# Kernel optimization log

Hardware: AMD Instinct MI355X
Metric: run time of the kernel (lower is better)

The kernel has to match this reference:

```python
import jax, jax.numpy as jnp
import numpy as np

N_NODES = 50000
N_EDGES = 400000
N_GRAPHS = 512
F = 32        # num_features
NB = 32       # mp_num_basis_fn
ZMAX = 118
CUTOFF = 5.0
NSPH = 9      # (mp_max_degree+1)^2 with max_degree=2
DEG_IDX = jnp.array([0, 1, 1, 1, 2, 2, 2, 2, 2])  # degree of each spherical component


def _bernstein(u, n=NB):
    # reciprocal_bernstein radial basis: Bernstein polynomials of degree n-1 at u in [0,1)
    k = jnp.arange(n, dtype=jnp.float32)
    log_binom = (jax.scipy.special.gammaln(float(n)) - jax.scipy.special.gammaln(k + 1.0)
                 - jax.scipy.special.gammaln(float(n) - k))
    u = jnp.clip(u, 1e-7, 1.0 - 1e-7)[..., None]
    return jnp.exp(log_binom + k * jnp.log(u) + (float(n) - 1.0 - k) * jnp.log1p(-u))


def _smooth_cutoff(r, cutoff=CUTOFF):
    t = r / cutoff
    return jnp.where(t < 1.0, jnp.exp(1.0 - 1.0 / jnp.clip(1.0 - t * t, 1e-7, None)), 0.0)


def _sph(u):
    # real spherical harmonics (cartesian normalization) up to degree 2; u: (E,3) unit vectors
    x, y, z = u[:, 0], u[:, 1], u[:, 2]
    c = jnp.sqrt(jnp.float32(3.0))
    return jnp.stack([jnp.ones_like(x), y, z, x,
                      c * x * y, c * y * z, 0.5 * (3.0 * z * z - 1.0),
                      c * z * x, 0.5 * c * (x * x - y * y)], axis=-1)


def _dense(x, W, b):
    # equivariant Dense: shared kernel over spherical components, bias only on scalar (l=0)
    y = jnp.einsum('nmf,fg->nmg', x, W)
    return y.at[:, 0, :].add(b)


def _silu_gate(x):
    # equivariant silu: scalar channel gates all degrees (scalar part -> exact silu)
    return x * jax.nn.sigmoid(x[:, 0:1, :])


def setup_inputs() -> dict:
    key = jax.random.key(0)
    ks = jax.random.split(key, 24)
    s = 1.0 / np.sqrt(F)
    sb = 1.0 / np.sqrt(NB)
    inp = {
        'positions': 2.0 * jax.random.normal(ks[0], (N_NODES, 3), jnp.float32),
        'embed': jax.random.normal(ks[1], (ZMAX, F), jnp.float32),
        'Wy0': sb * jax.random.normal(ks[2], (3, NB, F), jnp.float32),
        'Wx0': sb * jax.random.normal(ks[3], (3, NB, F), jnp.float32),
        'W1_0': s * jax.random.normal(ks[4], (F, F), jnp.float32),
        'b1_0': jnp.zeros((F,), jnp.float32),
        'W2_0': s * jax.random.normal(ks[5], (F, F), jnp.float32),
        'b2_0': jnp.zeros((F,), jnp.float32),
        'c0': jnp.full((1,), 0.5, jnp.float32),
        'Wr_last': sb * jax.random.normal(ks[6], (NB, F), jnp.float32),
        'W1_1': s * jax.random.normal(ks[7], (F, F), jnp.float32),
        'b1_1': jnp.zeros((F,), jnp.float32),
        'W2_1': s * jax.random.normal(ks[8], (F, F), jnp.float32),
        'b2_1': jnp.zeros((F,), jnp.float32),
        'c1': jnp.full((1,), 0.5, jnp.float32),
        'Wro1': s * jax.random.normal(ks[9], (F, F), jnp.float32),
        'bro1': jnp.zeros((F,), jnp.float32),
        'Wro2': s * jax.random.normal(ks[10], (F, 1), jnp.float32),
        'bro2': jnp.zeros((1,), jnp.float32),
        'atomic_bias': jax.random.normal(ks[11], (ZMAX,), jnp.float32),
        'atomic_numbers': jax.random.randint(ks[12], (N_NODES,), 0, ZMAX, jnp.int32),
        'dst_idx': jax.random.randint(ks[13], (N_EDGES,), 0, N_NODES, jnp.int32),
        'src_idx': jax.random.randint(ks[14], (N_EDGES,), 0, N_NODES, jnp.int32),
        'batch_segments': jnp.sort(jax.random.randint(ks[15], (N_NODES,), 0, N_GRAPHS, jnp.int32)),
        'graph_mask': jnp.ones((N_GRAPHS,), jnp.bool_),
    }
    return inp


def reference(positions, embed, Wy0, Wx0, W1_0, b1_0, W2_0, b2_0, c0,
              Wr_last, W1_1, b1_1, W2_1, b2_1, c1,
              Wro1, bro1, Wro2, bro2, atomic_bias,
              atomic_numbers, dst_idx, src_idx, batch_segments, graph_mask):
    # --- edge geometry (gather_src/gather_dst) ---
    disp = positions[src_idx] - positions[dst_idx]                # (E,3)
    r = jnp.sqrt(jnp.sum(disp * disp, axis=-1) + 1e-12)           # (E,)
    u = disp / r[:, None]
    Y = _sph(u)                                                   # (E,9)
    rbf = _bernstein(r / (r + 1.0)) * _smooth_cutoff(r)[:, None]  # (E,NB)

    # --- atomic embedding, lifted to (N, 9, F) with zero higher degrees ---
    x0 = embed[atomic_numbers]                                    # (N,F)
    x = jnp.concatenate([x0[:, None, :], jnp.zeros((N_NODES, NSPH - 1, F), x0.dtype)], axis=1)

    # --- iteration 0: full-degree equivariant message pass ---
    wy = jnp.einsum('eb,lbf->elf', rbf, Wy0)[:, DEG_IDX, :]       # (E,9,F) radial weights, (0,l)->l path
    wx = jnp.einsum('eb,lbf->elf', rbf, Wx0)[:, DEG_IDX, :]       # (l,0)->l path
    xs = x[src_idx]                                               # (E,9,F)
    msg = wy * Y[:, :, None] * xs[:, 0:1, :] + wx * xs
    y = jax.ops.segment_sum(msg, dst_idx, num_segments=N_NODES)   # (N,9,F)
    y = x + y
    y = _silu_gate(_dense(y, W1_0, b1_0))
    y = _dense(y, W2_0, b2_0)
    x = x + jax.nn.silu(c0) * y                                   # y_nl == 0 (era disabled)

    # --- iteration 1 (last): max_degree=0 message pass, then reduce to scalars ---
    w0 = rbf @ Wr_last                                            # (E,F)
    msg0 = w0 * x[src_idx, 0, :]
    y0 = jax.ops.segment_sum(msg0, dst_idx, num_segments=N_NODES) # (N,F)
    xs0 = x[:, 0, :]                                              # change_max_degree -> scalars
    y0 = xs0 + y0
    y0 = jax.nn.silu(y0 @ W1_1 + b1_1)
    y0 = y0 @ W2_1 + b2_1
    xs0 = xs0 + jax.nn.silu(c1) * y0

    # --- atomic readout and per-graph sum ---
    h = jax.nn.silu(xs0 @ Wro1 + bro1)
    e_atom = (h @ Wro2)[:, 0] + bro2[0] + atomic_bias[atomic_numbers]
    e_graph = jax.ops.segment_sum(e_atom, batch_segments, num_segments=N_GRAPHS)
    return jnp.where(graph_mask, e_graph, 0.0)
```

## Files before the change

kernel.cpp:

```cpp
#include <hip/hip_runtime.h>
#include <math.h>

#define NNODES 50000
#define NEDGES 400000
#define NGRAPHS 512
#define FDIM 32
#define CAP 32

static __device__ const float BINOM31[32] = {
    1.f, 31.f, 465.f, 4495.f, 31465.f, 169911.f, 736281.f, 2629575.f,
    7888725.f, 20160075.f, 44352165.f, 84672315.f, 141120525.f, 206253075.f,
    265182525.f, 300540195.f, 300540195.f, 265182525.f, 206253075.f,
    141120525.f, 84672315.f, 44352165.f, 20160075.f, 7888725.f, 2629575.f,
    736281.f, 169911.f, 31465.f, 4495.f, 465.f, 31.f, 1.f
};

__device__ __forceinline__ float fast_rcp(float x) {
    return __builtin_amdgcn_rcpf(x);
}
__device__ __forceinline__ float silu(float x) {
    return x * fast_rcp(1.0f + __expf(-x));
}

__global__ __launch_bounds__(256) void build_csr(
    const float* __restrict__ pos,
    const int* __restrict__ srci, const int* __restrict__ dsti,
    const int* __restrict__ Z,
    float4* __restrict__ pay, int* __restrict__ deg)
{
    int e = blockIdx.x * 256 + threadIdx.x;
    if (e >= NEDGES) return;
    int s = srci[e], d = dsti[e];
    float dx = pos[3 * s]     - pos[3 * d];
    float dy = pos[3 * s + 1] - pos[3 * d + 1];
    float dz = pos[3 * s + 2] - pos[3 * d + 2];
    float r = sqrtf(dx * dx + dy * dy + dz * dz + 1e-12f);
    if (r >= 5.0f) return;

    float t = r * 0.2f;
    float q = fmaxf(1.0f - t * t, 1e-7f);
    float cut = __expf(1.0f - fast_rcp(q));
    float v = fast_rcp(r + 1.0f);
    float v2 = v * v, v4 = v2 * v2, v8 = v4 * v4, v16 = v8 * v8;
    float scale = v16 * v8 * v4 * v2 * v * cut;

    int rank = atomicAdd(&deg[d], 1);
    if (rank < CAP)
        pay[(size_t)d * CAP + rank] =
            make_float4(r, scale,
                        __int_as_float(s * FDIM),
                        __int_as_float(Z[s] * FDIM));
}

#define GATHER_PIPE(ACC, XSRC, ROWSEL, CWL)                                \
    float ACC = 0.0f;                                                      \
    if (dgr > 0) {                                                         \
        float4 _pa = _h0, _pb = _h1;                                       \
        const float2* _cw = (const float2*)((CWL) + (f << 1));             \
        for (int j = 0; ; j += 2) {                                        \
            float _xa = (XSRC)[__float_as_int(_pa.ROWSEL) + f];            \
            float _xb = (XSRC)[__float_as_int(_pb.ROWSEL) + f];            \
            float4 _na = slot[j + 2];                                      \
            float4 _nb = slot[j + 3];                                      \
            float _r2a = _pa.x * _pa.x, _r2b = _pb.x * _pb.x;              \
            float2 _c15 = _cw[15 * 32];                                    \
            float _ea = _c15.x, _oa = _c15.y;                              \
            float _eb = _c15.x, _ob = _c15.y;                              \
            _Pragma("unroll")                                              \
            for (int p = 14; p >= 0; --p) {                                \
                float2 _cc = _cw[p * 32];                                  \
                _ea = fmaf(_ea, _r2a, _cc.x);                              \
                _oa = fmaf(_oa, _r2a, _cc.y);                              \
                _eb = fmaf(_eb, _r2b, _cc.x);                              \
                _ob = fmaf(_ob, _r2b, _cc.y);                              \
            }                                                              \
            float _wa = fmaf(_pa.x, _oa, _ea);                             \
            float _wb = fmaf(_pb.x, _ob, _eb);                             \
            ACC = fmaf(_pa.y * _wa, _xa, ACC);                             \
            ACC = fmaf(_pb.y * _wb, _xb, ACC);                             \
            if (j + 2 >= dgr) break;                                       \
            _pa = _na; _pb = _nb;                                          \
        }                                                                  \
    }

#define MATVEC32L(RES, WL, YP, BIAS) do {                                  \
    float4 _q0=(YP)[0], _q1=(YP)[1], _q2=(YP)[2], _q3=(YP)[3];             \
    float4 _q4=(YP)[4], _q5=(YP)[5], _q6=(YP)[6], _q7=(YP)[7];             \
    float _a0=(BIAS), _a1=0.f, _a2=0.f, _a3=0.f;                           \
    _a0=fmaf(_q0.x,(WL)[ 0*FDIM+f],_a0); _a0=fmaf(_q0.y,(WL)[ 1*FDIM+f],_a0); \
    _a0=fmaf(_q0.z,(WL)[ 2*FDIM+f],_a0); _a0=fmaf(_q0.w,(WL)[ 3*FDIM+f],_a0); \
    _a1=fmaf(_q1.x,(WL)[ 4*FDIM+f],_a1); _a1=fmaf(_q1.y,(WL)[ 5*FDIM+f],_a1); \
    _a1=fmaf(_q1.z,(WL)[ 6*FDIM+f],_a1); _a1=fmaf(_q1.w,(WL)[ 7*FDIM+f],_a1); \
    _a2=fmaf(_q2.x,(WL)[ 8*FDIM+f],_a2); _a2=fmaf(_q2.y,(WL)[ 9*FDIM+f],_a2); \
    _a2=fmaf(_q2.z,(WL)[10*FDIM+f],_a2); _a2=fmaf(_q2.w,(WL)[11*FDIM+f],_a2); \
    _a3=fmaf(_q3.x,(WL)[12*FDIM+f],_a3); _a3=fmaf(_q3.y,(WL)[13*FDIM+f],_a3); \
    _a3=fmaf(_q3.z,(WL)[14*FDIM+f],_a3); _a3=fmaf(_q3.w,(WL)[15*FDIM+f],_a3); \
    _a0=fmaf(_q4.x,(WL)[16*FDIM+f],_a0); _a0=fmaf(_q4.y,(WL)[17*FDIM+f],_a0); \
    _a0=fmaf(_q4.z,(WL)[18*FDIM+f],_a0); _a0=fmaf(_q4.w,(WL)[19*FDIM+f],_a0); \
    _a1=fmaf(_q5.x,(WL)[20*FDIM+f],_a1); _a1=fmaf(_q5.y,(WL)[21*FDIM+f],_a1); \
    _a1=fmaf(_q5.z,(WL)[22*FDIM+f],_a1); _a1=fmaf(_q5.w,(WL)[23*FDIM+f],_a1); \
    _a2=fmaf(_q6.x,(WL)[24*FDIM+f],_a2); _a2=fmaf(_q6.y,(WL)[25*FDIM+f],_a2); \
    _a2=fmaf(_q6.z,(WL)[26*FDIM+f],_a2); _a2=fmaf(_q6.w,(WL)[27*FDIM+f],_a2); \
    _a3=fmaf(_q7.x,(WL)[28*FDIM+f],_a3); _a3=fmaf(_q7.y,(WL)[29*FDIM+f],_a3); \
    _a3=fmaf(_q7.z,(WL)[30*FDIM+f],_a3); _a3=fmaf(_q7.w,(WL)[31*FDIM+f],_a3); \
    RES = (_a0+_a1)+(_a2+_a3); } while (0)

__global__ __launch_bounds__(256, 8) void fused_a(
    const float4* __restrict__ pay, const int* __restrict__ deg,
    const float* __restrict__ embed, const int* __restrict__ Z,
    const float* __restrict__ Wy0, const float* __restrict__ Wx0,
    const float* __restrict__ W1, const float* __restrict__ b1,
    const float* __restrict__ W2, const float* __restrict__ b2,
    const float* __restrict__ c0,
    float* __restrict__ x1buf)
{
    __shared__ __align__(16) float ylds[4][64];
    __shared__ __align__(16) float cwl[FDIM * FDIM];
    __shared__ __align__(16) float W1l[FDIM * FDIM];
    __shared__ __align__(16) float W2l[FDIM * FDIM];
    int tid = threadIdx.x;
    int widx = tid >> 6;
    int lane = tid & 63;
    int f    = lane & 31;
    int half = lane >> 5;

    int n = (blockIdx.x * 4 + widx) * 2 + half;
    const float4* slot = pay + (size_t)n * CAP;
    int dgr = (min(deg[n], CAP) + 1) & ~1;
    float4 _h0 = slot[0], _h1 = slot[1];
    float x0 = embed[Z[n] * FDIM + f];

    for (int i = tid; i < FDIM * FDIM; i += 256) {
        int k = i >> 5, ff = i & 31;
        cwl[(k >> 1) * 64 + (ff << 1) + (k & 1)] =
            BINOM31[k] * (Wy0[i] + Wx0[i]);
        W1l[i] = W1[i];
        W2l[i] = W2[i];
    }
    __syncthreads();

    GATHER_PIPE(accv, embed, w, cwl)

    float yv = x0 + accv;

    float* yrow = &ylds[widx][half * 32];
    const float4* yp = (const float4*)yrow;
    yrow[f] = yv;
    float t;
    MATVEC32L(t, W1l, yp, b1[f]);
    t = silu(t);
    yrow[f] = t;
    float u;
    MATVEC32L(u, W2l, yp, b2[f]);
    x1buf[(size_t)n * FDIM + f] = fmaf(silu(c0[0]), u, x0);
}

__global__ __launch_bounds__(256, 8) void fused_b(
    const float4* __restrict__ pay, const int* __restrict__ deg,
    const float* __restrict__ x1buf, const float* __restrict__ Wr_last,
    const float* __restrict__ W1, const float* __restrict__ b1,
    const float* __restrict__ W2, const float* __restrict__ b2,
    const float* __restrict__ c1,
    const float* __restrict__ Wro1, const float* __restrict__ bro1,
    const float* __restrict__ Wro2, const float* __restrict__ bro2,
    const float* __restrict__ abias, const int* __restrict__ Z,
    const int* __restrict__ segs,
    float* __restrict__ out)
{
    __shared__ __align__(16) float ylds[4][64];
    __shared__ __align__(16) float cwl[FDIM * FDIM];
    __shared__ __align__(16) float W1l[FDIM * FDIM];
    __shared__ __align__(16) float W2l[FDIM * FDIM];
    __shared__ __align__(16) float Wrl[FDIM * FDIM];
    __shared__ float eb[8];
    __shared__ int   sb[8];
    int tid = threadIdx.x;
    int widx = tid >> 6;
    int lane = tid & 63;
    int f    = lane & 31;
    int half = lane >> 5;

    int n = (blockIdx.x * 4 + widx) * 2 + half;
    const float4* slot = pay + (size_t)n * CAP;
    int dgr = (min(deg[n], CAP) + 1) & ~1;
    float4 _h0 = slot[0], _h1 = slot[1];
    float x1 = x1buf[(size_t)n * FDIM + f];
    int   zn = Z[n];

    for (int i = tid; i < FDIM * FDIM; i += 256) {
        int k = i >> 5, ff = i & 31;
        cwl[(k >> 1) * 64 + (ff << 1) + (k & 1)] = BINOM31[k] * Wr_last[i];
        W1l[i] = W1[i];
        W2l[i] = W2[i];
        Wrl[i] = Wro1[i];
    }
    __syncthreads();

    GATHER_PIPE(accv, x1buf, z, cwl)

    float yv = x1 + accv;

    float* yrow = &ylds[widx][half * 32];
    const float4* yp = (const float4*)yrow;
    yrow[f] = yv;
    float t;
    MATVEC32L(t, W1l, yp, b1[f]);
    t = silu(t);
    yrow[f] = t;
    float u;
    MATVEC32L(u, W2l, yp, b2[f]);
    float xs0 = fmaf(silu(c1[0]), u, x1);
    yrow[f] = xs0;
    float h;
    MATVEC32L(h, Wrl, yp, bro1[f]);
    float p = silu(h) * Wro2[f];
    p += __shfl_xor(p, 16, 32);
    p += __shfl_xor(p, 8, 32);
    p += __shfl_xor(p, 4, 32);
    p += __shfl_xor(p, 2, 32);
    p += __shfl_xor(p, 1, 32);

    if (f == 0) {
        eb[widx * 2 + half] = p + bro2[0] + abias[zn];
        sb[widx * 2 + half] = segs[n];
    }
    __syncthreads();
    if (tid == 0) {
        float acc = eb[0];
        int cur = sb[0];
        #pragma unroll
        for (int i = 1; i < 8; ++i) {
            if (sb[i] == cur) acc += eb[i];
            else { atomicAdd(&out[cur], acc); cur = sb[i]; acc = eb[i]; }
        }
        atomicAdd(&out[cur], acc);
    }
}

extern "C" void kernel_launch(void* const* d_in, const int* in_sizes, int n_in,
                              void* d_out, int out_size, void* d_ws, size_t ws_size,
                              hipStream_t stream)
{
    const float* pos     = (const float*)d_in[0];
    const float* embed   = (const float*)d_in[1];
    const float* Wy0     = (const float*)d_in[2];
    const float* Wx0     = (const float*)d_in[3];
    const float* W1_0    = (const float*)d_in[4];
    const float* b1_0    = (const float*)d_in[5];
    const float* W2_0    = (const float*)d_in[6];
    const float* b2_0    = (const float*)d_in[7];
    const float* c0      = (const float*)d_in[8];
    const float* Wr_last = (const float*)d_in[9];
    const float* W1_1    = (const float*)d_in[10];
    const float* b1_1    = (const float*)d_in[11];
    const float* W2_1    = (const float*)d_in[12];
    const float* b2_1    = (const float*)d_in[13];
    const float* c1      = (const float*)d_in[14];
    const float* Wro1    = (const float*)d_in[15];
    const float* bro1    = (const float*)d_in[16];
    const float* Wro2    = (const float*)d_in[17];
    const float* bro2    = (const float*)d_in[18];
    const float* abias   = (const float*)d_in[19];
    const int*   Z       = (const int*)d_in[20];
    const int*   dsti    = (const int*)d_in[21];
    const int*   srci    = (const int*)d_in[22];
    const int*   segs    = (const int*)d_in[23];

    float* out = (float*)d_out;

    char* w = (char*)d_ws;
    float4* pay   = (float4*)w;  w += (size_t)NNODES * CAP * 16;
    float*  x1buf = (float*)w;   w += (size_t)NNODES * FDIM * 4;
    int*    deg   = (int*)w;     w += (size_t)NNODES * 4;

    const int edgeBlocks = (NEDGES + 255) / 256;
    const int nodeBlocks = NNODES / 8;

    hipMemsetAsync(pay, 0, (size_t)NNODES * CAP * 16, stream);
    hipMemsetAsync(deg, 0, (size_t)NNODES * 4, stream);
    hipMemsetAsync(out, 0, (size_t)NGRAPHS * 4, stream);

    build_csr<<<edgeBlocks, 256, 0, stream>>>(pos, srci, dsti, Z, pay, deg);
    fused_a<<<nodeBlocks, 256, 0, stream>>>(pay, deg, embed, Z, Wy0, Wx0,
                                            W1_0, b1_0, W2_0, b2_0, c0, x1buf);
    fused_b<<<nodeBlocks, 256, 0, stream>>>(pay, deg, x1buf, Wr_last,
                                            W1_1, b1_1, W2_1, b2_1, c1,
                                            Wro1, bro1, Wro2, bro2,
                                            abias, Z, segs, out);
}
```

Baseline: 192.1 us.

## Make node kernels persistent with register-resident weights and in-loop segment accumulation

Result: no change. 189.2 us (-1.5%).

```diff
diff --git a/kernel.cpp b/kernel.cpp
--- a/kernel.cpp
+++ b/kernel.cpp
@@ -7,7 +7,11 @@
 #define FDIM 32
 #define CAP 32
 
-static __device__ const float BINOM31[32] = {
+#define NHALVES 4096
+#define NQ   (NNODES / NHALVES)
+#define NREM (NNODES % NHALVES)
+
+static constexpr float BINOM31[32] = {
     1.f, 31.f, 465.f, 4495.f, 31465.f, 169911.f, 736281.f, 2629575.f,
     7888725.f, 20160075.f, 44352165.f, 84672315.f, 141120525.f, 206253075.f,
     265182525.f, 300540195.f, 300540195.f, 265182525.f, 206253075.f,
@@ -52,27 +56,25 @@
                         __int_as_float(Z[s] * FDIM));
 }
 
-#define GATHER_PIPE(ACC, XSRC, ROWSEL, CWL)                                \
+#define GATHER_REG(ACC, XSRC, ROWSEL)                                      \
     float ACC = 0.0f;                                                      \
     if (dgr > 0) {                                                         \
-        float4 _pa = _h0, _pb = _h1;                                       \
-        const float2* _cw = (const float2*)((CWL) + (f << 1));             \
+        const float4* slot = pay + (size_t)n * CAP;                        \
+        float4 _pa = h0c, _pb = h1c;                                       \
         for (int j = 0; ; j += 2) {                                        \
             float _xa = (XSRC)[__float_as_int(_pa.ROWSEL) + f];            \
             float _xb = (XSRC)[__float_as_int(_pb.ROWSEL) + f];            \
             float4 _na = slot[j + 2];                                      \
             float4 _nb = slot[j + 3];                                      \
             float _r2a = _pa.x * _pa.x, _r2b = _pb.x * _pb.x;              \
-            float2 _c15 = _cw[15 * 32];                                    \
-            float _ea = _c15.x, _oa = _c15.y;                              \
-            float _eb = _c15.x, _ob = _c15.y;                              \
+            float _ea = cw[30], _oa = cw[31];                              \
+            float _eb = cw[30], _ob = cw[31];                              \
             _Pragma("unroll")                                              \
             for (int p = 14; p >= 0; --p) {                                \
-                float2 _cc = _cw[p * 32];                                  \
-                _ea = fmaf(_ea, _r2a, _cc.x);                              \
-                _oa = fmaf(_oa, _r2a, _cc.y);                              \
-                _eb = fmaf(_eb, _r2b, _cc.x);                              \
-                _ob = fmaf(_ob, _r2b, _cc.y);                              \
+                _ea = fmaf(_ea, _r2a, cw[2 * p]);                          \
+                _oa = fmaf(_oa, _r2a, cw[2 * p + 1]);                      \
+                _eb = fmaf(_eb, _r2b, cw[2 * p]);                          \
+                _ob = fmaf(_ob, _r2b, cw[2 * p + 1]);                      \
             }                                                              \
             float _wa = fmaf(_pa.x, _oa, _ea);                             \
             float _wb = fmaf(_pb.x, _ob, _eb);                             \
@@ -83,29 +85,35 @@
         }                                                                  \
     }
 
-#define MATVEC32L(RES, WL, YP, BIAS) do {                                  \
-    float4 _q0=(YP)[0], _q1=(YP)[1], _q2=(YP)[2], _q3=(YP)[3];             \
-    float4 _q4=(YP)[4], _q5=(YP)[5], _q6=(YP)[6], _q7=(YP)[7];             \
+#define MATVEC32R(RES, WR, BIAS) do {                                      \
+    float4 _q0=yp[0], _q1=yp[1], _q2=yp[2], _q3=yp[3];                     \
+    float4 _q4=yp[4], _q5=yp[5], _q6=yp[6], _q7=yp[7];                     \
     float _a0=(BIAS), _a1=0.f, _a2=0.f, _a3=0.f;                           \
-    _a0=fmaf(_q0.x,(WL)[ 0*FDIM+f],_a0); _a0=fmaf(_q0.y,(WL)[ 1*FDIM+f],_a0); \
-    _a0=fmaf(_q0.z,(WL)[ 2*FDIM+f],_a0); _a0=fmaf(_q0.w,(WL)[ 3*FDIM+f],_a0); \
-    _a1=fmaf(_q1.x,(WL)[ 4*FDIM+f],_a1); _a1=fmaf(_q1.y,(WL)[ 5*FDIM+f],_a1); \
-    _a1=fmaf(_q1.z,(WL)[ 6*FDIM+f],_a1); _a1=fmaf(_q1.w,(WL)[ 7*FDIM+f],_a1); \
-    _a2=fmaf(_q2.x,(WL)[ 8*FDIM+f],_a2); _a2=fmaf(_q2.y,(WL)[ 9*FDIM+f],_a2); \
-    _a2=fmaf(_q2.z,(WL)[10*FDIM+f],_a2); _a2=fmaf(_q2.w,(WL)[11*FDIM+f],_a2); \
-    _a3=fmaf(_q3.x,(WL)[12*FDIM+f],_a3); _a3=fmaf(_q3.y,(WL)[13*FDIM+f],_a3); \
-    _a3=fmaf(_q3.z,(WL)[14*FDIM+f],_a3); _a3=fmaf(_q3.w,(WL)[15*FDIM+f],_a3); \
-    _a0=fmaf(_q4.x,(WL)[16*FDIM+f],_a0); _a0=fmaf(_q4.y,(WL)[17*FDIM+f],_a0); \
-    _a0=fmaf(_q4.z,(WL)[18*FDIM+f],_a0); _a0=fmaf(_q4.w,(WL)[19*FDIM+f],_a0); \
-    _a1=fmaf(_q5.x,(WL)[20*FDIM+f],_a1); _a1=fmaf(_q5.y,(WL)[21*FDIM+f],_a1); \
-    _a1=fmaf(_q5.z,(WL)[22*FDIM+f],_a1); _a1=fmaf(_q5.w,(WL)[23*FDIM+f],_a1); \
-    _a2=fmaf(_q6.x,(WL)[24*FDIM+f],_a2); _a2=fmaf(_q6.y,(WL)[25*FDIM+f],_a2); \
-    _a2=fmaf(_q6.z,(WL)[26*FDIM+f],_a2); _a2=fmaf(_q6.w,(WL)[27*FDIM+f],_a2); \
-    _a3=fmaf(_q7.x,(WL)[28*FDIM+f],_a3); _a3=fmaf(_q7.y,(WL)[29*FDIM+f],_a3); \
-    _a3=fmaf(_q7.z,(WL)[30*FDIM+f],_a3); _a3=fmaf(_q7.w,(WL)[31*FDIM+f],_a3); \
+    _a0=fmaf(_q0.x,WR[ 0],_a0); _a0=fmaf(_q0.y,WR[ 1],_a0);                \
+    _a0=fmaf(_q0.z,WR[ 2],_a0); _a0=fmaf(_q0.w,WR[ 3],_a0);                \
+    _a1=fmaf(_q1.x,WR[ 4],_a1); _a1=fmaf(_q1.y,WR[ 5],_a1);                \
+    _a1=fmaf(_q1.z,WR[ 6],_a1); _a1=fmaf(_q1.w,WR[ 7],_a1);                \
+    _a2=fmaf(_q2.x,WR[ 8],_a2); _a2=fmaf(_q2.y,WR[ 9],_a2);                \
+    _a2=fmaf(_q2.z,WR[10],_a2); _a2=fmaf(_q2.w,WR[11],_a2);                \
+    _a3=fmaf(_q3.x,WR[12],_a3); _a3=fmaf(_q3.y,WR[13],_a3);                \
+    _a3=fmaf(_q3.z,WR[14],_a3); _a3=fmaf(_q3.w,WR[15],_a3);                \
+    _a0=fmaf(_q4.x,WR[16],_a0); _a0=fmaf(_q4.y,WR[17],_a0);                \
+    _a0=fmaf(_q4.z,WR[18],_a0); _a0=fmaf(_q4.w,WR[19],_a0);                \
+    _a1=fmaf(_q5.x,WR[20],_a1); _a1=fmaf(_q5.y,WR[21],_a1);                \
+    _a1=fmaf(_q5.z,WR[22],_a1); _a1=fmaf(_q5.w,WR[23],_a1);                \
+    _a2=fmaf(_q6.x,WR[24],_a2); _a2=fmaf(_q6.y,WR[25],_a2);                \
+    _a2=fmaf(_q6.z,WR[26],_a2); _a2=fmaf(_q6.w,WR[27],_a2);                \
+    _a3=fmaf(_q7.x,WR[28],_a3); _a3=fmaf(_q7.y,WR[29],_a3);                \
+    _a3=fmaf(_q7.z,WR[30],_a3); _a3=fmaf(_q7.w,WR[31],_a3);                \
     RES = (_a0+_a1)+(_a2+_a3); } while (0)
 
-__global__ __launch_bounds__(256, 8) void fused_a(
+__device__ __forceinline__ void half_range(int h, int& n0, int& n1) {
+    int a = h < NREM ? h * (NQ + 1) : NREM * (NQ + 1) + (h - NREM) * NQ;
+    n0 = a;
+    n1 = a + (h < NREM ? NQ + 1 : NQ);
+}
+
+__global__ __launch_bounds__(256, 2) void fused_a(
     const float4* __restrict__ pay, const int* __restrict__ deg,
     const float* __restrict__ embed, const int* __restrict__ Z,
     const float* __restrict__ Wy0, const float* __restrict__ Wx0,
@@ -115,47 +123,57 @@
     float* __restrict__ x1buf)
 {
     __shared__ __align__(16) float ylds[4][64];
-    __shared__ __align__(16) float cwl[FDIM * FDIM];
-    __shared__ __align__(16) float W1l[FDIM * FDIM];
-    __shared__ __align__(16) float W2l[FDIM * FDIM];
     int tid = threadIdx.x;
     int widx = tid >> 6;
     int lane = tid & 63;
     int f    = lane & 31;
     int half = lane >> 5;
 
-    int n = (blockIdx.x * 4 + widx) * 2 + half;
-    const float4* slot = pay + (size_t)n * CAP;
-    int dgr = (min(deg[n], CAP) + 1) & ~1;
-    float4 _h0 = slot[0], _h1 = slot[1];
-    float x0 = embed[Z[n] * FDIM + f];
-
-    for (int i = tid; i < FDIM * FDIM; i += 256) {
-        int k = i >> 5, ff = i & 31;
-        cwl[(k >> 1) * 64 + (ff << 1) + (k & 1)] =
-            BINOM31[k] * (Wy0[i] + Wx0[i]);
-        W1l[i] = W1[i];
-        W2l[i] = W2[i];
-    }
-    __syncthreads();
-
-    GATHER_PIPE(accv, embed, w, cwl)
-
-    float yv = x0 + accv;
+    float cw[32], w1r[32], w2r[32];
+    #pragma unroll
+    for (int k = 0; k < 32; ++k) {
+        cw[k]  = BINOM31[k] * (Wy0[k * FDIM + f] + Wx0[k * FDIM + f]);
+        w1r[k] = W1[k * FDIM + f];
+        w2r[k] = W2[k * FDIM + f];
+    }
+    float b1f = b1[f], b2f = b2[f];
+    float sc0 = silu(c0[0]);
+
+    int hidx = (blockIdx.x * 4 + widx) * 2 + half;
+    int n0, n1;
+    half_range(hidx, n0, n1);
 
     float* yrow = &ylds[widx][half * 32];
     const float4* yp = (const float4*)yrow;
-    yrow[f] = yv;
-    float t;
-    MATVEC32L(t, W1l, yp, b1[f]);
-    t = silu(t);
-    yrow[f] = t;
-    float u;
-    MATVEC32L(u, W2l, yp, b2[f]);
-    x1buf[(size_t)n * FDIM + f] = fmaf(silu(c0[0]), u, x0);
-}
-
-__global__ __launch_bounds__(256, 8) void fused_b(
+
+    int dgr = min(deg[n0], CAP);
+    const float4* sl0 = pay + (size_t)n0 * CAP;
+    float4 h0c = sl0[0], h1c = sl0[1];
+    float x0 = embed[Z[n0] * FDIM + f];
+
+    for (int n = n0; n < n1; ++n) {
+        GATHER_REG(accv, embed, w)
+
+        int nn = (n + 1 < n1) ? n + 1 : n;
+        int dgr_n = min(deg[nn], CAP);
+        const float4* sln = pay + (size_t)nn * CAP;
+        float4 h0n = sln[0], h1n = sln[1];
+        float x0n = embed[Z[nn] * FDIM + f];
+
+        yrow[f] = x0 + accv;
+        float t;
+        MATVEC32R(t, w1r, b1f);
+        t = silu(t);
+        yrow[f] = t;
+        float u;
+        MATVEC32R(u, w2r, b2f);
+        x1buf[(size_t)n * FDIM + f] = fmaf(sc0, u, x0);
+
+        dgr = dgr_n; h0c = h0n; h1c = h1n; x0 = x0n;
+    }
+}
+
+__global__ __launch_bounds__(256, 2) void fused_b(
     const float4* __restrict__ pay, const int* __restrict__ deg,
     const float* __restrict__ x1buf, const float* __restrict__ Wr_last,
     const float* __restrict__ W1, const float* __restrict__ b1,
@@ -168,73 +186,82 @@
     float* __restrict__ out)
 {
     __shared__ __align__(16) float ylds[4][64];
-    __shared__ __align__(16) float cwl[FDIM * FDIM];
-    __shared__ __align__(16) float W1l[FDIM * FDIM];
-    __shared__ __align__(16) float W2l[FDIM * FDIM];
-    __shared__ __align__(16) float Wrl[FDIM * FDIM];
-    __shared__ float eb[8];
-    __shared__ int   sb[8];
     int tid = threadIdx.x;
     int widx = tid >> 6;
     int lane = tid & 63;
     int f    = lane & 31;
     int half = lane >> 5;
 
-    int n = (blockIdx.x * 4 + widx) * 2 + half;
-    const float4* slot = pay + (size_t)n * CAP;
-    int dgr = (min(deg[n], CAP) + 1) & ~1;
-    float4 _h0 = slot[0], _h1 = slot[1];
-    float x1 = x1buf[(size_t)n * FDIM + f];
-    int   zn = Z[n];
-
-    for (int i = tid; i < FDIM * FDIM; i += 256) {
-        int k = i >> 5, ff = i & 31;
-        cwl[(k >> 1) * 64 + (ff << 1) + (k & 1)] = BINOM31[k] * Wr_last[i];
-        W1l[i] = W1[i];
-        W2l[i] = W2[i];
-        Wrl[i] = Wro1[i];
-    }
-    __syncthreads();
-
-    GATHER_PIPE(accv, x1buf, z, cwl)
-
-    float yv = x1 + accv;
+    float cw[32], w1r[32], w2r[32], wrr[32];
+    #pragma unroll
+    for (int k = 0; k < 32; ++k) {
+        cw[k]  = BINOM31[k] * Wr_last[k * FDIM + f];
+        w1r[k] = W1[k * FDIM + f];
+        w2r[k] = W2[k * FDIM + f];
+        wrr[k] = Wro1[k * FDIM + f];
+    }
+    float b1f = b1[f], b2f = b2[f], bro1f = bro1[f], wro2f = Wro2[f];
+    float sc1 = silu(c1[0]);
+    float bro2v = bro2[0];
+
+    int hidx = (blockIdx.x * 4 + widx) * 2 + half;
+    int n0, n1;
+    half_range(hidx, n0, n1);
 
     float* yrow = &ylds[widx][half * 32];
     const float4* yp = (const float4*)yrow;
-    yrow[f] = yv;
-    float t;
-    MATVEC32L(t, W1l, yp, b1[f]);
-    t = silu(t);
-    yrow[f] = t;
-    float u;
-    MATVEC32L(u, W2l, yp, b2[f]);
-    float xs0 = fmaf(silu(c1[0]), u, x1);
-    yrow[f] = xs0;
-    float h;
-    MATVEC32L(h, Wrl, yp, bro1[f]);
-    float p = silu(h) * Wro2[f];
-    p += __shfl_xor(p, 16, 32);
-    p += __shfl_xor(p, 8, 32);
-    p += __shfl_xor(p, 4, 32);
-    p += __shfl_xor(p, 2, 32);
-    p += __shfl_xor(p, 1, 32);
-
-    if (f == 0) {
-        eb[widx * 2 + half] = p + bro2[0] + abias[zn];
-        sb[widx * 2 + half] = segs[n];
-    }
-    __syncthreads();
-    if (tid == 0) {
-        float acc = eb[0];
-        int cur = sb[0];
-        #pragma unroll
-        for (int i = 1; i < 8; ++i) {
-            if (sb[i] == cur) acc += eb[i];
-            else { atomicAdd(&out[cur], acc); cur = sb[i]; acc = eb[i]; }
+
+    int dgr = min(deg[n0], CAP);
+    const float4* sl0 = pay + (size_t)n0 * CAP;
+    float4 h0c = sl0[0], h1c = sl0[1];
+    float x1 = x1buf[(size_t)n0 * FDIM + f];
+    float ab = abias[Z[n0]];
+    int   sg = segs[n0];
+
+    float segacc = 0.0f;
+    int   curseg = -1;
+
+    for (int n = n0; n < n1; ++n) {
+        GATHER_REG(accv, x1buf, z)
+
+        int nn = (n + 1 < n1) ? n + 1 : n;
+        int dgr_n = min(deg[nn], CAP);
+        const float4* sln = pay + (size_t)nn * CAP;
+        float4 h0n = sln[0], h1n = sln[1];
+        float x1n = x1buf[(size_t)nn * FDIM + f];
+        float abn = abias[Z[nn]];
+        int   sgn = segs[nn];
+
+        yrow[f] = x1 + accv;
+        float t;
+        MATVEC32R(t, w1r, b1f);
+        t = silu(t);
+        yrow[f] = t;
+        float u;
+        MATVEC32R(u, w2r, b2f);
+        float xs0 = fmaf(sc1, u, x1);
+        yrow[f] = xs0;
+        float h;
+        MATVEC32R(h, wrr, bro1f);
+        float p = silu(h) * wro2f;
+        p += __shfl_xor(p, 16, 32);
+        p += __shfl_xor(p, 8, 32);
+        p += __shfl_xor(p, 4, 32);
+        p += __shfl_xor(p, 2, 32);
+        p += __shfl_xor(p, 1, 32);
+
+        if (f == 0) {
+            float e = p + bro2v + ab;
+            if (sg == curseg) segacc += e;
+            else {
+                if (curseg >= 0) atomicAdd(&out[curseg], segacc);
+                curseg = sg; segacc = e;
+            }
         }
-        atomicAdd(&out[cur], acc);
-    }
+
+        dgr = dgr_n; h0c = h0n; h1c = h1n; x1 = x1n; ab = abn; sg = sgn;
+    }
+    if (f == 0 && curseg >= 0) atomicAdd(&out[curseg], segacc);
 }
 
 extern "C" void kernel_launch(void* const* d_in, const int* in_sizes, int n_in,
@@ -274,16 +301,16 @@
     int*    deg   = (int*)w;     w += (size_t)NNODES * 4;
 
     const int edgeBlocks = (NEDGES + 255) / 256;
-    const int nodeBlocks = NNODES / 8;
+    const int persBlocks = NHALVES / 8;
 
     hipMemsetAsync(pay, 0, (size_t)NNODES * CAP * 16, stream);
     hipMemsetAsync(deg, 0, (size_t)NNODES * 4, stream);
     hipMemsetAsync(out, 0, (size_t)NGRAPHS * 4, stream);
 
     build_csr<<<edgeBlocks, 256, 0, stream>>>(pos, srci, dsti, Z, pay, deg);
-    fused_a<<<nodeBlocks, 256, 0, stream>>>(pay, deg, embed, Z, Wy0, Wx0,
+    fused_a<<<persBlocks, 256, 0, stream>>>(pay, deg, embed, Z, Wy0, Wx0,
                                             W1_0, b1_0, W2_0, b2_0, c0, x1buf);
-    fused_b<<<nodeBlocks, 256, 0, stream>>>(pay, deg, x1buf, Wr_last,
+    fused_b<<<persBlocks, 256, 0, stream>>>(pay, deg, x1buf, Wr_last,
                                             W1_1, b1_1, W2_1, b2_1, c1,
                                             Wro1, bro1, Wro2, bro2,
                                             abias, Z, segs, out);
```
